# Kernel optimization log

Measured on AMD Instinct MI355X. Metric: run time of the kernel, lower is better.

The kernel has to match this reference:

```python
import jax, jax.numpy as jnp
import numpy as np

D_MODEL = 1024
N_HEADS = 16
HEAD_DIM = D_MODEL // N_HEADS


def setup_inputs() -> dict:
    key = jax.random.key(0)
    k1, k2, k3 = jax.random.split(key, 3)
    scale = 0.02
    x = jax.random.normal(k1, (2, 2048, D_MODEL), dtype=jnp.float32)
    w_qkv = jax.random.normal(k2, (D_MODEL, 3 * D_MODEL), dtype=jnp.float32) * scale
    b_qkv = jnp.zeros((3 * D_MODEL,), dtype=jnp.float32)
    w_proj = jax.random.normal(k3, (D_MODEL, D_MODEL), dtype=jnp.float32) * scale
    b_proj = jnp.zeros((D_MODEL,), dtype=jnp.float32)
    return {"x": x, "w_qkv": w_qkv, "b_qkv": b_qkv, "w_proj": w_proj, "b_proj": b_proj}


def reference(x, w_qkv, b_qkv, w_proj, b_proj):
    bsz, seq_len, d_model = x.shape
    qkv = x @ w_qkv + b_qkv  # [B,S,3D]
    q, k, v = jnp.split(qkv, 3, axis=-1)
    # [B,S,D] -> [B,H,S,hd]
    def to_heads(t):
        return t.reshape(bsz, seq_len, N_HEADS, HEAD_DIM).transpose(0, 2, 1, 3)
    q, k, v = to_heads(q), to_heads(k), to_heads(v)
    scores = jnp.einsum("bhqd,bhkd->bhqk", q, k) / jnp.sqrt(jnp.float32(HEAD_DIM))
    causal = jnp.triu(jnp.ones((seq_len, seq_len), dtype=bool), k=1)
    scores = jnp.where(causal, -jnp.inf, scores)
    attn = jax.nn.softmax(scores, axis=-1)
    out = jnp.einsum("bhqk,bhkd->bhqd", attn, v)  # [B,H,S,hd]
    out = out.transpose(0, 2, 1, 3).reshape(bsz, seq_len, d_model)
    return out @ w_proj + b_proj
```

## Files before the change

### kernel.cpp

```cpp
#include <hip/hip_runtime.h>
#include <hip/hip_bf16.h>

#define D_MODEL 1024
#define SEQ     2048
#define NH      16
#define HD      64
#define M_TOK   4096
#define THREE_D 3072

using bf16x8 = __bf16 __attribute__((ext_vector_type(8)));
using bf16x4 = __bf16 __attribute__((ext_vector_type(4)));
using f32x4  = float  __attribute__((ext_vector_type(4)));

typedef __attribute__((address_space(3))) uint32_t lds_u32;
typedef const __attribute__((address_space(1))) uint32_t glb_u32;

__global__ __launch_bounds__(256) void cast_kernel(const float* __restrict__ in,
                                                   __bf16* __restrict__ out, int n4) {
  int i = blockIdx.x * 256 + threadIdx.x;
  if (i < n4) {
    float4 f = reinterpret_cast<const float4*>(in)[i];
    bf16x4 o;
    o[0] = (__bf16)f.x; o[1] = (__bf16)f.y; o[2] = (__bf16)f.z; o[3] = (__bf16)f.w;
    reinterpret_cast<bf16x4*>(out)[i] = o;
  }
}

__global__ __launch_bounds__(256) void transpose_cast(const float* __restrict__ in,
                                                      __bf16* __restrict__ out, int R, int C) {
  __shared__ float tile[64][65];
  int c0 = blockIdx.x * 64, r0 = blockIdx.y * 64;
  int tx = threadIdx.x & 63, ty = threadIdx.x >> 6;
#pragma unroll
  for (int i = 0; i < 16; ++i) {
    int r = ty + i * 4;
    tile[r][tx] = in[(size_t)(r0 + r) * C + c0 + tx];
  }
  __syncthreads();
#pragma unroll
  for (int i = 0; i < 16; ++i) {
    int r = ty + i * 4;
    out[(size_t)(c0 + r) * R + r0 + tx] = (__bf16)tile[tx][r];
  }
}

template <int EPI>
__global__ __launch_bounds__(256, 2) void gemm_bt(const __bf16* __restrict__ A,
                                                  const __bf16* __restrict__ BT,
                                                  const float* __restrict__ bias,
                                                  int Kdim, int Ncols,
                                                  __bf16* __restrict__ qb, __bf16* __restrict__ kb,
                                                  __bf16* __restrict__ vb, float* __restrict__ fout) {
  __shared__ __bf16 As[128 * 32];
  __shared__ __bf16 Bs[128 * 32];
  const int tid  = threadIdx.x;
  const int lane = tid & 63, wave = tid >> 6;
  const int lr = lane & 15, lg = lane >> 4;
  const int wm = (wave >> 1) * 64, wn = (wave & 1) * 64;
  const int m0 = blockIdx.y * 128, n0 = blockIdx.x * 128;
  const int srow = tid >> 2, scol = (tid & 3) * 8;

  f32x4 acc[4][4] = {};

  const __bf16* aSrc = A  + (size_t)(m0 + srow) * Kdim + scol;
  const __bf16* bSrc = BT + (size_t)(n0 + srow) * Kdim + scol;
  __bf16* aDst = As + wave * 512;
  __bf16* bDst = Bs + wave * 512;

  for (int k0 = 0; k0 < Kdim; k0 += 32) {
    __syncthreads();
    __builtin_amdgcn_global_load_lds((glb_u32*)(aSrc + k0),              (lds_u32*)aDst,          16, 0, 0);
    __builtin_amdgcn_global_load_lds((glb_u32*)(aSrc + 64 * Kdim + k0), (lds_u32*)(aDst + 2048), 16, 0, 0);
    __builtin_amdgcn_global_load_lds((glb_u32*)(bSrc + k0),              (lds_u32*)bDst,          16, 0, 0);
    __builtin_amdgcn_global_load_lds((glb_u32*)(bSrc + 64 * Kdim + k0), (lds_u32*)(bDst + 2048), 16, 0, 0);
    asm volatile("s_waitcnt vmcnt(0)" ::: "memory");
    __syncthreads();

    bf16x8 af[4], bfv[4];
#pragma unroll
    for (int i = 0; i < 4; ++i) af[i]  = *reinterpret_cast<const bf16x8*>(&As[(wm + i * 16 + lr) * 32 + lg * 8]);
#pragma unroll
    for (int j = 0; j < 4; ++j) bfv[j] = *reinterpret_cast<const bf16x8*>(&Bs[(wn + j * 16 + lr) * 32 + lg * 8]);
#pragma unroll
    for (int i = 0; i < 4; ++i)
#pragma unroll
      for (int j = 0; j < 4; ++j)
        acc[i][j] = __builtin_amdgcn_mfma_f32_16x16x32_bf16(af[i], bfv[j], acc[i][j], 0, 0, 0);
  }

#pragma unroll
  for (int i = 0; i < 4; ++i) {
#pragma unroll
    for (int j = 0; j < 4; ++j) {
      const int gc = n0 + wn + j * 16 + lr;
      const float bv = bias[gc];
#pragma unroll
      for (int ii = 0; ii < 4; ++ii) {
        const int gr = m0 + wm + i * 16 + lg * 4 + ii;
        float val = acc[i][j][ii] + bv;
        if (EPI == 0) {
          int t = gc >> 10, rem = gc & 1023;
          int h = rem >> 6, d = rem & 63;
          int b = gr >> 11, s = gr & 2047;
          if (t == 0) {
            qb[(((size_t)(b * NH + h)) * SEQ + s) * HD + d] = (__bf16)(val * 0.125f);
          } else if (t == 1) {
            kb[(((size_t)(b * NH + h)) * SEQ + s) * HD + d] = (__bf16)val;
          } else {
            vb[(((size_t)(b * NH + h)) * HD + d) * SEQ + s] = (__bf16)val;
          }
        } else {
          fout[(size_t)gr * Ncols + gc] = val;
        }
      }
    }
  }
}

__global__ __launch_bounds__(256, 4) void attn_kernel(const __bf16* __restrict__ Q,
                                                      const __bf16* __restrict__ K,
                                                      const __bf16* __restrict__ VT,
                                                      __bf16* __restrict__ AO) {
  __shared__ __bf16 Kb[2][64 * 64];
  __shared__ __bf16 Vb[2][64 * 64];
  __shared__ __bf16 Ps[4][16 * 64];

  const int tid  = threadIdx.x;
  const int lane = tid & 63, wave = tid >> 6;
  const int lr = lane & 15, lg = lane >> 4;

  const int f    = blockIdx.x;
  const int c    = f & 7;
  const int u    = f >> 3;
  const int bh   = c * 4 + (u & 3);
  const int qblk = 31 - (u >> 2);

  const int q0 = qblk * 64 + wave * 16;
  const size_t base = (size_t)bh * SEQ * HD;
  const char* Kg  = (const char*)(K + base);
  const char* VTg = (const char*)(VT + base);

  bf16x8 qf[2];
#pragma unroll
  for (int kc = 0; kc < 2; ++kc)
    qf[kc] = *reinterpret_cast<const bf16x8*>(Q + base + (size_t)(q0 + lr) * HD + kc * 32 + lg * 8);

  float lrun[4] = {0.f, 0.f, 0.f, 0.f};
  f32x4 o[4] = {};

  const int nt = qblk + 1;
  const int nmaxF = (wave | 1) + 1;

  auto stage = [&](int bufp, int t) {
    const int k0 = t * 64;
#pragma unroll
    for (int p = 0; p < 2; ++p) {
      const int row = wave * 16 + p * 8 + (lane >> 3);
      {
        const int srcOff = (k0 + row) * 128 + (((lane & 7) ^ (row & 7)) << 4);
        __builtin_amdgcn_global_load_lds((glb_u32*)(Kg + srcOff),
                                         (lds_u32*)&Kb[bufp][(wave * 16 + p * 8) * 64], 16, 0, 0);
      }
      {
        const int srcOff = row * 4096 + k0 * 2 + (((lane & 7) ^ (row & 7)) << 4);
        __builtin_amdgcn_global_load_lds((glb_u32*)(VTg + srcOff),
                                         (lds_u32*)&Vb[bufp][(wave * 16 + p * 8) * 64], 16, 0, 0);
      }
    }
  };

  stage(0, 0);
  asm volatile("s_waitcnt vmcnt(0)" ::: "memory");
  __syncthreads();

  for (int t = 0; t < nt; ++t) {
    const int p = t & 1;
    const int k0 = t * 64;
    const bool last = (t == nt - 1);
    const int nmax = last ? nmaxF : 4;
    const int kcmax = nmax >> 1;

    if (t + 1 < nt) stage(p ^ 1, t + 1);

    const __bf16* Kt = Kb[p];
    const __bf16* Vt = Vb[p];

    f32x4 s[4] = {};
#pragma unroll
    for (int kc = 0; kc < 2; ++kc) {
#pragma unroll
      for (int n = 0; n < 4; ++n)
        if (n < nmax) {
          bf16x8 kf = *reinterpret_cast<const bf16x8*>(
              &Kt[(n * 16 + lr) * 64 + (((kc * 4 + lg) ^ (lr & 7)) << 3)]);
          s[n] = __builtin_amdgcn_mfma_f32_16x16x32_bf16(qf[kc], kf, s[n], 0, 0, 0);
        }
    }

    if (last) {
#pragma unroll
      for (int n = 0; n < 4; ++n)
        if (n < nmax)
#pragma unroll
          for (int ii = 0; ii < 4; ++ii) {
            int qg = q0 + lg * 4 + ii;
            int kg = k0 + n * 16 + lr;
            if (kg > qg) s[n][ii] = -__builtin_inff();
          }
    }

#pragma unroll
    for (int n = 0; n < 4; ++n)
      if (n < nmax)
#pragma unroll
        for (int ii = 0; ii < 4; ++ii) {
          float pv = __expf(s[n][ii]);
          lrun[ii] += pv;
          const int row = lg * 4 + ii;
          Ps[wave][row * 64 + (((n * 2 + (lr >> 3)) ^ (row & 7)) << 3) + (lr & 7)] = (__bf16)pv;
        }

#pragma unroll
    for (int kc = 0; kc < 2; ++kc)
      if (kc < kcmax) {
        bf16x8 pa = *reinterpret_cast<const bf16x8*>(
            &Ps[wave][lr * 64 + (((kc * 4 + lg) ^ (lr & 7)) << 3)]);
#pragma unroll
        for (int nd = 0; nd < 4; ++nd) {
          bf16x8 vf = *reinterpret_cast<const bf16x8*>(
              &Vt[(nd * 16 + lr) * 64 + (((kc * 4 + lg) ^ (lr & 7)) << 3)]);
          o[nd] = __builtin_amdgcn_mfma_f32_16x16x32_bf16(pa, vf, o[nd], 0, 0, 0);
        }
      }

    asm volatile("s_waitcnt vmcnt(0)" ::: "memory");
    __syncthreads();
  }

#pragma unroll
  for (int off = 1; off <= 8; off <<= 1)
#pragma unroll
    for (int ii = 0; ii < 4; ++ii) lrun[ii] += __shfl_xor(lrun[ii], off, 64);

  const int b = bh >> 4, h = bh & 15;
  float rl[4];
#pragma unroll
  for (int ii = 0; ii < 4; ++ii) rl[ii] = 1.f / lrun[ii];
#pragma unroll
  for (int nd = 0; nd < 4; ++nd)
#pragma unroll
    for (int ii = 0; ii < 4; ++ii) {
      int row = q0 + lg * 4 + ii;
      AO[((size_t)(b * SEQ) + row) * D_MODEL + h * HD + nd * 16 + lr] = (__bf16)(o[nd][ii] * rl[ii]);
    }
}

extern "C" void kernel_launch(void* const* d_in, const int* in_sizes, int n_in,
                              void* d_out, int out_size, void* d_ws, size_t ws_size,
                              hipStream_t stream) {
  const float* x      = (const float*)d_in[0];
  const float* w_qkv  = (const float*)d_in[1];
  const float* b_qkv  = (const float*)d_in[2];
  const float* w_proj = (const float*)d_in[3];
  const float* b_proj = (const float*)d_in[4];
  float* out = (float*)d_out;

  char* ws = (char*)d_ws;
  __bf16* xb     = (__bf16*)(ws);
  __bf16* wqkvT  = (__bf16*)(ws + 8388608);
  __bf16* wprojT = (__bf16*)(ws + 14680064);
  __bf16* qb     = (__bf16*)(ws + 16777216);
  __bf16* kb     = (__bf16*)(ws + 25165824);
  __bf16* vtb    = (__bf16*)(ws + 33554432);
  __bf16* ao     = (__bf16*)(ws + 41943040);

  cast_kernel<<<4096, 256, 0, stream>>>(x, xb, M_TOK * D_MODEL / 4);
  transpose_cast<<<dim3(THREE_D / 64, D_MODEL / 64), 256, 0, stream>>>(w_qkv, wqkvT, D_MODEL, THREE_D);
  transpose_cast<<<dim3(D_MODEL / 64, D_MODEL / 64), 256, 0, stream>>>(w_proj, wprojT, D_MODEL, D_MODEL);

  gemm_bt<0><<<dim3(THREE_D / 128, M_TOK / 128), 256, 0, stream>>>(
      xb, wqkvT, b_qkv, D_MODEL, THREE_D, qb, kb, vtb, nullptr);

  attn_kernel<<<1024, 256, 0, stream>>>(qb, kb, vtb, ao);

  gemm_bt<1><<<dim3(D_MODEL / 128, M_TOK / 128), 256, 0, stream>>>(
      ao, wprojT, b_proj, D_MODEL, D_MODEL, nullptr, nullptr, nullptr, out);
}
```

Measured before the change: 121.8 us.

## Split GEMM into specialized QKV and proj kernels, reorder attention block schedule

Replaces the templated GEMM with a dedicated QKV kernel (compile-time K, hoisted head index math, occupancy hint raised to 3) and a projection GEMM using 64x128 tiles, which doubles the grid to 512 blocks so all CUs get work. The attention kernel's query-block ordering is changed to interleave long and short causal blocks across scheduling groups to balance load. Smaller projection tiles reduce reuse per block, and the higher occupancy hint may constrain registers.

```diff
diff --git a/kernel.cpp b/kernel.cpp
--- a/kernel.cpp
+++ b/kernel.cpp
@@ -44,15 +44,14 @@
   }
 }
 
-template <int EPI>
-__global__ __launch_bounds__(256, 2) void gemm_bt(const __bf16* __restrict__ A,
-                                                  const __bf16* __restrict__ BT,
-                                                  const float* __restrict__ bias,
-                                                  int Kdim, int Ncols,
-                                                  __bf16* __restrict__ qb, __bf16* __restrict__ kb,
-                                                  __bf16* __restrict__ vb, float* __restrict__ fout) {
+__global__ __launch_bounds__(256, 3) void gemm_qkv(const __bf16* __restrict__ A,
+                                                   const __bf16* __restrict__ BT,
+                                                   const float* __restrict__ bias,
+                                                   __bf16* __restrict__ qb, __bf16* __restrict__ kb,
+                                                   __bf16* __restrict__ vb) {
   __shared__ __bf16 As[128 * 32];
   __shared__ __bf16 Bs[128 * 32];
+  const int Kdim = D_MODEL;
   const int tid  = threadIdx.x;
   const int lane = tid & 63, wave = tid >> 6;
   const int lr = lane & 15, lg = lane >> 4;
@@ -94,24 +93,76 @@
     for (int j = 0; j < 4; ++j) {
       const int gc = n0 + wn + j * 16 + lr;
       const float bv = bias[gc];
+      const int t = gc >> 10, rem = gc & 1023;
+      const int h = rem >> 6, d = rem & 63;
 #pragma unroll
       for (int ii = 0; ii < 4; ++ii) {
         const int gr = m0 + wm + i * 16 + lg * 4 + ii;
-        float val = acc[i][j][ii] + bv;
-        if (EPI == 0) {
-          int t = gc >> 10, rem = gc & 1023;
-          int h = rem >> 6, d = rem & 63;
-          int b = gr >> 11, s = gr & 2047;
-          if (t == 0) {
-            qb[(((size_t)(b * NH + h)) * SEQ + s) * HD + d] = (__bf16)(val * 0.125f);
-          } else if (t == 1) {
-            kb[(((size_t)(b * NH + h)) * SEQ + s) * HD + d] = (__bf16)val;
-          } else {
-            vb[(((size_t)(b * NH + h)) * HD + d) * SEQ + s] = (__bf16)val;
-          }
+        const float val = acc[i][j][ii] + bv;
+        const int b = gr >> 11, s = gr & 2047;
+        if (t == 0) {
+          qb[(((size_t)(b * NH + h)) * SEQ + s) * HD + d] = (__bf16)(val * 0.125f);
+        } else if (t == 1) {
+          kb[(((size_t)(b * NH + h)) * SEQ + s) * HD + d] = (__bf16)val;
         } else {
-          fout[(size_t)gr * Ncols + gc] = val;
+          vb[(((size_t)(b * NH + h)) * HD + d) * SEQ + s] = (__bf16)val;
         }
+      }
+    }
+  }
+}
+
+__global__ __launch_bounds__(256, 4) void gemm_proj(const __bf16* __restrict__ A,
+                                                    const __bf16* __restrict__ BT,
+                                                    const float* __restrict__ bias,
+                                                    float* __restrict__ fout) {
+  __shared__ __bf16 As[64 * 32];
+  __shared__ __bf16 Bs[128 * 32];
+  const int Kdim = D_MODEL;
+  const int tid  = threadIdx.x;
+  const int lane = tid & 63, wave = tid >> 6;
+  const int lr = lane & 15, lg = lane >> 4;
+  const int wm = (wave >> 1) * 32, wn = (wave & 1) * 64;
+  const int n0 = blockIdx.x * 128, m0 = blockIdx.y * 64;
+  const int srow = tid >> 2, scol = (tid & 3) * 8;
+
+  f32x4 acc[2][4] = {};
+
+  const __bf16* aSrc = A  + (size_t)(m0 + srow) * Kdim + scol;
+  const __bf16* bSrc = BT + (size_t)(n0 + srow) * Kdim + scol;
+  __bf16* aDst = As + wave * 512;
+  __bf16* bDst = Bs + wave * 512;
+
+  for (int k0 = 0; k0 < Kdim; k0 += 32) {
+    __syncthreads();
+    __builtin_amdgcn_global_load_lds((glb_u32*)(aSrc + k0),              (lds_u32*)aDst,          16, 0, 0);
+    __builtin_amdgcn_global_load_lds((glb_u32*)(bSrc + k0),              (lds_u32*)bDst,          16, 0, 0);
+    __builtin_amdgcn_global_load_lds((glb_u32*)(bSrc + 64 * Kdim + k0), (lds_u32*)(bDst + 2048), 16, 0, 0);
+    asm volatile("s_waitcnt vmcnt(0)" ::: "memory");
+    __syncthreads();
+
+    bf16x8 af[2], bfv[4];
+#pragma unroll
+    for (int i = 0; i < 2; ++i) af[i]  = *reinterpret_cast<const bf16x8*>(&As[(wm + i * 16 + lr) * 32 + lg * 8]);
+#pragma unroll
+    for (int j = 0; j < 4; ++j) bfv[j] = *reinterpret_cast<const bf16x8*>(&Bs[(wn + j * 16 + lr) * 32 + lg * 8]);
+#pragma unroll
+    for (int i = 0; i < 2; ++i)
+#pragma unroll
+      for (int j = 0; j < 4; ++j)
+        acc[i][j] = __builtin_amdgcn_mfma_f32_16x16x32_bf16(af[i], bfv[j], acc[i][j], 0, 0, 0);
+  }
+
+#pragma unroll
+  for (int i = 0; i < 2; ++i) {
+#pragma unroll
+    for (int j = 0; j < 4; ++j) {
+      const int gc = n0 + wn + j * 16 + lr;
+      const float bv = bias[gc];
+#pragma unroll
+      for (int ii = 0; ii < 4; ++ii) {
+        const int gr = m0 + wm + i * 16 + lg * 4 + ii;
+        fout[(size_t)gr * D_MODEL + gc] = acc[i][j][ii] + bv;
       }
     }
   }
@@ -129,11 +180,12 @@
   const int lane = tid & 63, wave = tid >> 6;
   const int lr = lane & 15, lg = lane >> 4;
 
-  const int f    = blockIdx.x;
-  const int c    = f & 7;
-  const int u    = f >> 3;
-  const int bh   = c * 4 + (u & 3);
-  const int qblk = 31 - (u >> 2);
+  const int f  = blockIdx.x;
+  const int c  = f & 7;
+  const int u  = f >> 3;
+  const int bh = c * 4 + (u & 3);
+  const int s2 = u >> 2, grp = s2 >> 3, r = s2 & 7;
+  const int qblk = (grp == 0) ? (31 - r) : (grp == 1) ? r : (grp == 2) ? (39 - s2) : (s2 - 16);
 
   const int q0 = qblk * 64 + wave * 16;
   const size_t base = (size_t)bh * SEQ * HD;
@@ -278,11 +330,11 @@
   transpose_cast<<<dim3(THREE_D / 64, D_MODEL / 64), 256, 0, stream>>>(w_qkv, wqkvT, D_MODEL, THREE_D);
   transpose_cast<<<dim3(D_MODEL / 64, D_MODEL / 64), 256, 0, stream>>>(w_proj, wprojT, D_MODEL, D_MODEL);
 
-  gemm_bt<0><<<dim3(THREE_D / 128, M_TOK / 128), 256, 0, stream>>>(
-      xb, wqkvT, b_qkv, D_MODEL, THREE_D, qb, kb, vtb, nullptr);
+  gemm_qkv<<<dim3(THREE_D / 128, M_TOK / 128), 256, 0, stream>>>(
+      xb, wqkvT, b_qkv, qb, kb, vtb);
 
   attn_kernel<<<1024, 256, 0, stream>>>(qb, kb, vtb, ao);
 
-  gemm_bt<1><<<dim3(D_MODEL / 128, M_TOK / 128), 256, 0, stream>>>(
-      ao, wprojT, b_proj, D_MODEL, D_MODEL, nullptr, nullptr, nullptr, out);
-}
+  gemm_proj<<<dim3(D_MODEL / 128, M_TOK / 64), 256, 0, stream>>>(
+      ao, wprojT, b_proj, out);
+}
```

Result: faster. 114.8 us (-5.8%).
